# Optimization experiments

Measured on AMD Instinct MI355X. Metric: run time of the kernel, lower is better.

Reference implementation:

```python
import jax, jax.numpy as jnp
import numpy as np
from jax import lax


def conv(x, w, b, stride, pad):
    # x: [B,C,H,W], w: [O,I,kh,kw] (torch layout)
    y = lax.conv_general_dilated(x, w, (stride, stride), ((pad, pad), (pad, pad)),
                                 dimension_numbers=('NCHW', 'OIHW', 'NCHW'))
    return y + b[None, :, None, None]


def convT(x, w, b, stride, pad):
    # torch ConvTranspose2d weight layout [in, out, kh, kw]
    k = w.shape[2]
    wf = jnp.flip(w, (2, 3)).transpose(1, 0, 2, 3)  # -> [out, in, kh, kw]
    p = k - 1 - pad
    y = lax.conv_general_dilated(x, wf, (1, 1), ((p, p), (p, p)),
                                 lhs_dilation=(stride, stride),
                                 dimension_numbers=('NCHW', 'OIHW', 'NCHW'))
    return y + b[None, :, None, None]


def resblock(x, wa, ba, wb, bb):
    h = conv(jax.nn.relu(x), wa, ba, 1, 1)   # 3x3
    h2 = conv(jax.nn.relu(h), wb, bb, 1, 0)  # 1x1
    return x + h2


def vqvae_forward(x, e1_w, e1_b, e2_w, e2_b, e3_w, e3_b,
                  er1a_w, er1a_b, er1b_w, er1b_b, er2a_w, er2a_b, er2b_w, er2b_b,
                  codebook,
                  d1_w, d1_b, dr1a_w, dr1a_b, dr1b_w, dr1b_b,
                  dr2a_w, dr2a_b, dr2b_w, dr2b_b,
                  dt1_w, dt1_b, dt2_w, dt2_b):
    # encoder
    h = jax.nn.relu(conv(x, e1_w, e1_b, 2, 1))
    h = jax.nn.relu(conv(h, e2_w, e2_b, 2, 1))
    h = conv(h, e3_w, e3_b, 1, 1)
    h = resblock(h, er1a_w, er1a_b, er1b_w, er1b_b)
    ze = resblock(h, er2a_w, er2a_b, er2b_w, er2b_b)  # [B,C,H,W]
    # VQ: nearest codebook vector per spatial location (squared L2)
    zef = ze.transpose(0, 2, 3, 1)  # [B,H,W,C]
    # ||z - e||^2 = ||z||^2 - 2 z.e + ||e||^2 (same argmin as explicit broadcast)
    d = (jnp.sum(zef * zef, -1, keepdims=True)
         - 2.0 * jnp.einsum('bhwc,kc->bhwk', zef, codebook)
         + jnp.sum(codebook * codebook, -1))  # [B,H,W,K]
    idx = jnp.argmin(d, -1)                    # [B,H,W]
    zq = codebook[idx].transpose(0, 3, 1, 2)   # [B,C,H,W]
    # straight-through estimator
    dec_in = ze + lax.stop_gradient(zq - ze)
    # decoder
    g = conv(dec_in, d1_w, d1_b, 1, 1)
    g = resblock(g, dr1a_w, dr1a_b, dr1b_w, dr1b_b)
    g = resblock(g, dr2a_w, dr2a_b, dr2b_w, dr2b_b)
    g = jax.nn.relu(convT(g, dt1_w, dt1_b, 2, 1))
    x_hat = convT(g, dt2_w, dt2_b, 2, 1)
    return x_hat, ze, zq


def setup_inputs() -> dict:
    key = jax.random.key(0)
    ks = iter(jax.random.split(key, 64))
    C, K = 128, 512

    def w(shape, scale=0.02):
        return jax.random.normal(next(ks), shape, jnp.float32) * scale

    inp = {}
    inp['x'] = jax.random.normal(next(ks), (16, 3, 256, 256), jnp.float32)
    inp['e1_w'] = w((C, 3, 4, 4)); inp['e1_b'] = w((C,))
    inp['e2_w'] = w((C, C, 4, 4)); inp['e2_b'] = w((C,))
    inp['e3_w'] = w((C, C, 3, 3)); inp['e3_b'] = w((C,))
    inp['er1a_w'] = w((C, C, 3, 3)); inp['er1a_b'] = w((C,))
    inp['er1b_w'] = w((C, C, 1, 1)); inp['er1b_b'] = w((C,))
    inp['er2a_w'] = w((C, C, 3, 3)); inp['er2a_b'] = w((C,))
    inp['er2b_w'] = w((C, C, 1, 1)); inp['er2b_b'] = w((C,))
    inp['codebook'] = jax.random.uniform(next(ks), (K, C), jnp.float32, -1.0 / K, 1.0 / K)
    inp['d1_w'] = w((C, C, 3, 3)); inp['d1_b'] = w((C,))
    inp['dr1a_w'] = w((C, C, 3, 3)); inp['dr1a_b'] = w((C,))
    inp['dr1b_w'] = w((C, C, 1, 1)); inp['dr1b_b'] = w((C,))
    inp['dr2a_w'] = w((C, C, 3, 3)); inp['dr2a_b'] = w((C,))
    inp['dr2b_w'] = w((C, C, 1, 1)); inp['dr2b_b'] = w((C,))
    inp['dt1_w'] = w((C, C, 4, 4)); inp['dt1_b'] = w((C,))   # ConvTranspose [in,out,kh,kw]
    inp['dt2_w'] = w((C, 3, 4, 4)); inp['dt2_b'] = w((3,))
    return inp


def reference(x, e1_w, e1_b, e2_w, e2_b, e3_w, e3_b,
              er1a_w, er1a_b, er1b_w, er1b_b, er2a_w, er2a_b, er2b_w, er2b_b,
              codebook,
              d1_w, d1_b, dr1a_w, dr1a_b, dr1b_w, dr1b_b,
              dr2a_w, dr2a_b, dr2b_w, dr2b_b,
              dt1_w, dt1_b, dt2_w, dt2_b):
    return vqvae_forward(x, e1_w, e1_b, e2_w, e2_b, e3_w, e3_b,
                         er1a_w, er1a_b, er1b_w, er1b_b, er2a_w, er2a_b, er2b_w, er2b_b,
                         codebook,
                         d1_w, d1_b, dr1a_w, dr1a_b, dr1b_w, dr1b_b,
                         dr2a_w, dr2a_b, dr2b_w, dr2b_b,
                         dt1_w, dt1_b, dt2_w, dt2_b)
```

## Files before the change

### kernel.cpp

```cpp
#include <hip/hip_runtime.h>
#include <stdint.h>

typedef unsigned short u16;
typedef __attribute__((ext_vector_type(8))) short short8;
typedef __attribute__((ext_vector_type(4))) float floatx4;

#define RS66  (66*128)
#define IS66  (66*66*128)
#define RS130 (130*128)
#define IS130 (130*130*128)

__device__ __forceinline__ float bf2f(u16 h) {
  union { unsigned u; float f; } v; v.u = ((unsigned)h) << 16; return v.f;
}
__device__ __forceinline__ u16 f2bf(float f) {
  union { float f; unsigned u; } v; v.f = f;
  unsigned r = v.u + 0x7FFFu + ((v.u >> 16) & 1u);
  return (u16)(r >> 16);
}
__device__ __forceinline__ void gl_lds16(const void* g, void* l) {
  __builtin_amdgcn_global_load_lds(
      (const __attribute__((address_space(1))) void*)(uintptr_t)g,
      (__attribute__((address_space(3))) void*)(uintptr_t)l, 16, 0, 0);
}
__device__ __forceinline__ unsigned fkey(float f) {
  unsigned u = __float_as_uint(f);
  return (u & 0x80000000u) ? ~u : (u | 0x80000000u);
}

struct Taps { int n; unsigned dh2; unsigned dw2; };

__global__ __launch_bounds__(256) void conv_mfma(
    const u16* __restrict__ in, int inRS, int inIS, int si,
    const u16* __restrict__ wt, const float* __restrict__ bias, Taps tp,
    u16* __restrict__ out, int outRS, int outIS, int so, int oh0, int ow0,
    const u16* __restrict__ res, u16* __restrict__ out2, int reluMain,
    float* __restrict__ zeFc, u16* __restrict__ zeBFc, int multi)
{
  __shared__ u16 lA[4096];
  __shared__ u16 lB[4096];
  const int tid = threadIdx.x;
  const int w = tid >> 6, lane = tid & 63, quad = lane >> 4, l16 = lane & 15;
  const int wm = w >> 1, wn = w & 1;
  const int q = tid & 3, p0 = tid >> 2;
  const int blockM = blockIdx.x << 7;

  unsigned dh2 = tp.dh2, dw2 = tp.dw2;
  if (multi) {
    const int cls = blockIdx.y;
    dh2 = (tp.dh2 >> (8*cls)) & 0xffu;
    dw2 = (tp.dw2 >> (8*cls)) & 0xffu;
    wt += cls << 16;
    oh0 = cls >> 1; ow0 = cls & 1;
  }

  const int pg0 = blockM + p0, pg1 = pg0 + 64;
  const int b0 = pg0 >> 12, mo0 = (pg0 >> 6) & 63, no0 = pg0 & 63;
  const int b1 = pg1 >> 12, mo1 = (pg1 >> 6) & 63, no1 = pg1 & 63;
  const u16* gA0 = in + b0*inIS + si*mo0*inRS + si*no0*128 + q*8;
  const u16* gA1 = in + b1*inIS + si*mo1*inRS + si*no1*128 + q*8;
  const u16* gB0 = wt + p0*128 + q*8;
  const u16* gB1 = gB0 + 64*128;
  u16* lsA0 = lA + w*512; u16* lsA1 = lsA0 + 2048;
  u16* lsB0 = lB + w*512; u16* lsB1 = lsB0 + 2048;

  floatx4 zz = {0.f,0.f,0.f,0.f};
  floatx4 acc[4][4];
#pragma unroll
  for (int i=0;i<4;i++)
#pragma unroll
    for (int j=0;j<4;j++) acc[i][j] = zz;

  for (int t = 0; t < tp.n; ++t) {
    const int dh = (int)((dh2 >> (2*t)) & 3u) - 1;
    const int dw = (int)((dw2 >> (2*t)) & 3u) - 1;
    const int aoff = dh*inRS + dw*128;
    const int boff = t << 14;
#pragma unroll
    for (int kc = 0; kc < 4; ++kc) {
      __syncthreads();
      gl_lds16(gA0 + aoff + kc*32, lsA0);
      gl_lds16(gA1 + aoff + kc*32, lsA1);
      gl_lds16(gB0 + boff + kc*32, lsB0);
      gl_lds16(gB1 + boff + kc*32, lsB1);
      __syncthreads();
      short8 af[4], bfr[4];
#pragma unroll
      for (int s=0;s<4;s++) af[s]  = *(const short8*)&lA[(wm*64 + s*16 + l16)*32 + quad*8];
#pragma unroll
      for (int s=0;s<4;s++) bfr[s] = *(const short8*)&lB[(wn*64 + s*16 + l16)*32 + quad*8];
#pragma unroll
      for (int i=0;i<4;i++)
#pragma unroll
        for (int j=0;j<4;j++)
          acc[i][j] = __builtin_amdgcn_mfma_f32_16x16x32_bf16(af[i], bfr[j], acc[i][j], 0, 0, 0);
    }
  }

  float bv[4];
#pragma unroll
  for (int j=0;j<4;j++) bv[j] = bias[wn*64 + j*16 + l16];

#pragma unroll
  for (int i=0;i<4;i++) {
#pragma unroll
    for (int r=0;r<4;r++) {
      const int p = blockM + wm*64 + i*16 + quad*4 + r;
      const int bb = p >> 12, mo = (p >> 6) & 63, no = p & 63;
      const int ob = bb*outIS + (so*mo + oh0)*outRS + (so*no + ow0)*128;
#pragma unroll
      for (int j=0;j<4;j++) {
        const int n = wn*64 + j*16 + l16;
        float v = acc[i][j][r] + bv[j];
        if (res)  v += bf2f(res[ob + n]);
        if (out)  out[ob + n]  = f2bf(reluMain ? fmaxf(v, 0.f) : v);
        if (out2) out2[ob + n] = f2bf(fmaxf(v, 0.f));
        if (zeFc) {
          zeFc[((size_t)p << 7) + n] = v;
          zeBFc[((size_t)p << 7) + n] = f2bf(v);
        }
      }
    }
  }
}

__global__ __launch_bounds__(256) void vq_score(
    const u16* __restrict__ zeBF, const u16* __restrict__ cbBF,
    const float* __restrict__ cbn, unsigned long long* __restrict__ minbuf)
{
  __shared__ u16 lA[4096];
  __shared__ u16 lB[4096];
  const int tid = threadIdx.x;
  const int w = tid >> 6, lane = tid & 63, quad = lane >> 4, l16 = lane & 15;
  const int wm = w >> 1, wn = w & 1;
  const int q = tid & 3, p0 = tid >> 2;
  const int blockM = blockIdx.x << 7;
  const int nb = blockIdx.y;
  const u16* gA0 = zeBF + ((blockM + p0) << 7) + q*8;
  const u16* gA1 = gA0 + (64 << 7);
  const u16* gB0 = cbBF + ((nb*128 + p0) << 7) + q*8;
  const u16* gB1 = gB0 + (64 << 7);
  u16* lsA0 = lA + w*512; u16* lsA1 = lsA0 + 2048;
  u16* lsB0 = lB + w*512; u16* lsB1 = lsB0 + 2048;

  floatx4 zz = {0.f,0.f,0.f,0.f};
  floatx4 acc[4][4];
#pragma unroll
  for (int i=0;i<4;i++)
#pragma unroll
    for (int j=0;j<4;j++) acc[i][j] = zz;

#pragma unroll
  for (int kc = 0; kc < 4; ++kc) {
    __syncthreads();
    gl_lds16(gA0 + kc*32, lsA0);
    gl_lds16(gA1 + kc*32, lsA1);
    gl_lds16(gB0 + kc*32, lsB0);
    gl_lds16(gB1 + kc*32, lsB1);
    __syncthreads();
    short8 af[4], bfr[4];
#pragma unroll
    for (int s=0;s<4;s++) af[s]  = *(const short8*)&lA[(wm*64 + s*16 + l16)*32 + quad*8];
#pragma unroll
    for (int s=0;s<4;s++) bfr[s] = *(const short8*)&lB[(wn*64 + s*16 + l16)*32 + quad*8];
#pragma unroll
    for (int i=0;i<4;i++)
#pragma unroll
      for (int j=0;j<4;j++)
        acc[i][j] = __builtin_amdgcn_mfma_f32_16x16x32_bf16(af[i], bfr[j], acc[i][j], 0, 0, 0);
  }

  float cn[4];
#pragma unroll
  for (int j=0;j<4;j++) cn[j] = cbn[nb*128 + wn*64 + j*16 + l16];

#pragma unroll
  for (int i=0;i<4;i++) {
#pragma unroll
    for (int r=0;r<4;r++) {
      const int p = blockM + wm*64 + i*16 + quad*4 + r;
      unsigned long long best = 0xFFFFFFFFFFFFFFFFull;
#pragma unroll
      for (int j=0;j<4;j++) {
        const int n = nb*128 + wn*64 + j*16 + l16;
        float v = cn[j] - acc[i][j][r];
        unsigned long long pk = ((unsigned long long)fkey(v) << 32) | (unsigned)n;
        if (pk < best) best = pk;
      }
#pragma unroll
      for (int d=1; d<16; d<<=1) {
        unsigned long long o = __shfl_xor(best, d, 64);
        if (o < best) best = o;
      }
      if (l16 == 0) atomicMin(minbuf + p, best);
    }
  }
}

__global__ __launch_bounds__(256) void finalize(
    const float* __restrict__ zeFc, const unsigned long long* __restrict__ minb,
    const float* __restrict__ cb, float* __restrict__ outZe, float* __restrict__ outZq,
    u16* __restrict__ zqI)
{
  __shared__ float T[64*129];
  __shared__ int ns[64];
  const int tid = threadIdx.x;
  const int P0 = blockIdx.x << 6;
  const int b = P0 >> 12, hw0 = P0 & 4095;

#pragma unroll
  for (int it=0; it<32; ++it) {
    int e = it*256 + tid;
    int px = e >> 7, c = e & 127;
    T[px*129 + c] = zeFc[((size_t)P0 << 7) + e];
  }
  if (tid < 64) ns[tid] = (int)(unsigned)(minb[P0 + tid] & 0xFFFFFFFFull);
  __syncthreads();

  float* zeB = outZe + (((size_t)b) << 19) + hw0;
  float* zqB = outZq + (((size_t)b) << 19) + hw0;
  const int h = hw0 >> 6;
  u16* zqIB = zqI + b*IS66 + h*RS66;
#pragma unroll
  for (int it=0; it<32; ++it) {
    const int c = it*4 + (tid >> 6);
    const int px = tid & 63;
    zeB[(c << 12) + px] = T[px*129 + c];
    float v = cb[(ns[px] << 7) + c];
    zqB[(c << 12) + px] = v;
    zqIB[px*128 + c] = f2bf(v);
  }
}

__global__ __launch_bounds__(256) void zero_halos(
    u16* big, u16* s0, u16* s1, u16* s2, u16* s3, unsigned long long* minb)
{
  int id = blockIdx.x*256 + threadIdx.x;
  if (id >= 463872) return;
  if (id >= 398336) { minb[id - 398336] = 0xFFFFFFFFFFFFFFFFull; return; }
  u16* base; int H, W;
  if (id < 132096) { base = big; H = 128; W = 128; }
  else {
    id -= 132096;
    int bi = id / 66560;
    id -= bi*66560;
    base = (bi == 0) ? s0 : (bi == 1) ? s1 : (bi == 2) ? s2 : s3;
    H = 64; W = 64;
  }
  int Wp = W+2, Hp = H+2;
  int cv = id & 15; int rest = id >> 4;
  int npx = 2*Wp + 2*H;
  int img = rest / npx; int pix = rest - img*npx;
  int hh, wwp;
  if (pix < Wp) { hh = 0; wwp = pix; }
  else if (pix < 2*Wp) { hh = Hp-1; wwp = pix - Wp; }
  else { int r2 = pix - 2*Wp; hh = 1 + (r2 >> 1); wwp = (r2 & 1) ? (Wp-1) : 0; }
  uint4 zv = {0u,0u,0u,0u};
  *(uint4*)(base + (((size_t)img*Hp + hh)*Wp + wwp)*128 + cv*8) = zv;
}

struct WEnt { const float* src; u16* dst; int O, I, T, mode; };
struct WTab { int n; WEnt e[16]; int cum[17]; };
__global__ __launch_bounds__(256) void prep_w(WTab wt) {
  int id = blockIdx.x*256 + threadIdx.x;
  if (id >= wt.cum[wt.n]) return;
  int k = 0;
  while (id >= wt.cum[k+1]) k++;
  int l = id - wt.cum[k];
  WEnt E = wt.e[k];
  if (E.mode == 0) {
    int i = l % E.I; int rest = l / E.I; int o = rest % E.O; int t = rest / E.O;
    E.dst[l] = f2bf(E.src[(o*E.I + i)*E.T + t]);
  } else if (E.mode == 1) {
    int i = l & 127, o = (l >> 7) & 127, tt = (l >> 14) & 3, cls = l >> 16;
    int th = tt >> 1, tw = tt & 1, po = cls >> 1, pw = cls & 1;
    int kh = po ? (th ? 2 : 0) : (th ? 3 : 1);
    int kw = pw ? (tw ? 2 : 0) : (tw ? 3 : 1);
    E.dst[l] = f2bf(E.src[((i*128 + o)*4 + kh)*4 + kw]);
  } else if (E.mode == 2) {
    E.dst[l] = f2bf(E.src[l]);
  } else if (E.mode == 3) {
    float s = 0.f; const float* r = E.src + l*128;
    for (int c=0;c<128;c++) s += r[c]*r[c];
    ((float*)E.dst)[l] = 0.5f*s;
  } else if (E.mode == 4) {
    int o = l & 127, tap = l >> 7;
    ((float*)E.dst)[l] = E.src[o*48 + tap];
  } else {
    int c = l & 127, n = l >> 7;
    int o = n >> 4, kk = n & 15;
    E.dst[l] = f2bf(E.src[c*48 + o*16 + kk]);
  }
}

__global__ __launch_bounds__(256) void conv_e1(
    const float* __restrict__ x, const float* __restrict__ wT,
    const float* __restrict__ bias, u16* __restrict__ outI)
{
  __shared__ float inS[12*260];
  __shared__ float wS[48*128];
  __shared__ float bS[128];
  const int tid = threadIdx.x;
  const int b = blockIdx.x >> 7, ho = blockIdx.x & 127;

  for (int l = tid; l < 1536; l += 256)
    ((float4*)wS)[l] = ((const float4*)wT)[l];
  if (tid < 128) bS[tid] = bias[tid];
  for (int l = tid; l < 3120; l += 256) {
    int col = l % 260; int rest = l / 260;
    int kh = rest & 3, c = rest >> 2;
    int hi = 2*ho + kh - 1, wi = col - 1;
    float v = 0.f;
    if ((unsigned)hi < 256u && (unsigned)wi < 256u)
      v = x[((b*3 + c) << 16) + (hi << 8) + wi];
    inS[rest*260 + col] = v;
  }
  __syncthreads();

  const int g = tid & 7;
  const int pxg = tid >> 3;
  floatx4 acc[4][4];
  {
    const floatx4* bp = (const floatx4*)&bS[g*16];
    floatx4 b0 = bp[0], b1 = bp[1], b2 = bp[2], b3 = bp[3];
#pragma unroll
    for (int px=0;px<4;px++) { acc[px][0]=b0; acc[px][1]=b1; acc[px][2]=b2; acc[px][3]=b3; }
  }
#pragma unroll
  for (int c=0;c<3;c++)
#pragma unroll
    for (int kh=0;kh<4;kh++) {
      const float* row = &inS[(c*4+kh)*260];
#pragma unroll
      for (int kw=0;kw<4;kw++) {
        const int tap = c*16 + kh*4 + kw;
        const floatx4* wp = (const floatx4*)&wS[tap*128 + g*16];
        floatx4 w0 = wp[0], w1 = wp[1], w2 = wp[2], w3 = wp[3];
#pragma unroll
        for (int px=0;px<4;px++) {
          float xv = row[((pxg*4 + px) << 1) + kw];
          acc[px][0] += xv*w0; acc[px][1] += xv*w1;
          acc[px][2] += xv*w2; acc[px][3] += xv*w3;
        }
      }
    }

  u16* ob = outI + b*IS130 + ho*RS130;
#pragma unroll
  for (int px=0;px<4;px++) {
    const int wo = pxg*4 + px;
    u16* p = ob + wo*128 + g*16;
#pragma unroll
    for (int k=0;k<4;k++) {
      union { u16 u[4]; uint2 v2; } pk;
#pragma unroll
      for (int j=0;j<4;j++) pk.u[j] = f2bf(fmaxf(acc[px][k][j], 0.f));
      *(uint2*)(p + k*4) = pk.v2;
    }
  }
}

__global__ __launch_bounds__(256) void dt2_gemm(
    const u16* __restrict__ inI, const u16* __restrict__ Wb,
    float* __restrict__ cols)
{
  const int tid = threadIdx.x;
  const int w = tid >> 6, lane = tid & 63, quad = lane >> 4, l16 = lane & 15;
  const int pixBase = blockIdx.x*256 + w*64;

  short8 Bf[3][4];
#pragma unroll
  for (int nt=0; nt<3; nt++)
#pragma unroll
    for (int kc=0; kc<4; kc++)
      Bf[nt][kc] = *(const short8*)(Wb + (nt*16 + l16)*128 + kc*32 + quad*8);

  const u16* ap[4];
#pragma unroll
  for (int ms=0; ms<4; ms++) {
    int p = pixBase + ms*16 + l16;
    int b = p >> 14, rem = p & 16383;
    ap[ms] = inI + b*IS130 + (rem >> 7)*RS130 + (rem & 127)*128;
  }

  floatx4 zz = {0.f,0.f,0.f,0.f};
  floatx4 acc[4][3];
#pragma unroll
  for (int ms=0; ms<4; ms++)
#pragma unroll
    for (int nt=0; nt<3; nt++) acc[ms][nt] = zz;

#pragma unroll
  for (int kc=0; kc<4; kc++) {
#pragma unroll
    for (int ms=0; ms<4; ms++) {
      short8 a = *(const short8*)(ap[ms] + kc*32 + quad*8);
#pragma unroll
      for (int nt=0; nt<3; nt++)
        acc[ms][nt] = __builtin_amdgcn_mfma_f32_16x16x32_bf16(a, Bf[nt][kc], acc[ms][nt], 0, 0, 0);
    }
  }

#pragma unroll
  for (int ms=0; ms<4; ms++)
#pragma unroll
    for (int nt=0; nt<3; nt++)
#pragma unroll
      for (int r=0; r<4; r++) {
        int p = pixBase + ms*16 + quad*4 + r;
        cols[(size_t)p*48 + nt*16 + l16] = acc[ms][nt][r];
      }
}

__global__ __launch_bounds__(256) void dt2_gather(
    const float* __restrict__ cols, const float* __restrict__ bias,
    float* __restrict__ xhat)
{
  int id = blockIdx.x*256 + threadIdx.x;
  int b = id >> 16, rem = id & 65535;
  int ho = rem >> 8, wo = rem & 255;
  const int ph = ho & 1, pw = wo & 1;
  const int hi0 = ph ? ((ho+1)>>1) : (ho>>1);
  const int kh0 = ph ? 0 : 1;
  const int wi0 = pw ? ((wo+1)>>1) : (wo>>1);
  const int kw0 = pw ? 0 : 1;
  float a0 = bias[0], a1 = bias[1], a2 = bias[2];
#pragma unroll
  for (int th=0; th<2; th++) {
    const int hi = hi0 - th;
    if ((unsigned)hi >= 128u) continue;
    const int kh = kh0 + 2*th;
#pragma unroll
    for (int tw=0; tw<2; tw++) {
      const int wi = wi0 - tw;
      if ((unsigned)wi >= 128u) continue;
      const int kw = kw0 + 2*tw;
      const float* r = cols + (size_t)((b << 14) + (hi << 7) + wi)*48 + (kh*4 + kw);
      a0 += r[0]; a1 += r[16]; a2 += r[32];
    }
  }
  const int ob = ((b*3) << 16) + (ho << 8) + wo;
  xhat[ob]          = a0;
  xhat[ob + 65536]  = a1;
  xhat[ob + 131072] = a2;
}

extern "C" void kernel_launch(void* const* d_in, const int* in_sizes, int n_in,
                              void* d_out, int out_size, void* d_ws, size_t ws_size,
                              hipStream_t stream)
{
  const float* x     = (const float*)d_in[0];
  const float* e1w   = (const float*)d_in[1];
  const float* e1b   = (const float*)d_in[2];
  const float* e2w   = (const float*)d_in[3];
  const float* e2b   = (const float*)d_in[4];
  const float* e3w   = (const float*)d_in[5];
  const float* e3b   = (const float*)d_in[6];
  const float* er1aw = (const float*)d_in[7];
  const float* er1ab = (const float*)d_in[8];
  const float* er1bw = (const float*)d_in[9];
  const float* er1bb = (const float*)d_in[10];
  const float* er2aw = (const float*)d_in[11];
  const float* er2ab = (const float*)d_in[12];
  const float* er2bw = (const float*)d_in[13];
  const float* er2bb = (const float*)d_in[14];
  const float* cb    = (const float*)d_in[15];
  const float* d1w   = (const float*)d_in[16];
  const float* d1b   = (const float*)d_in[17];
  const float* dr1aw = (const float*)d_in[18];
  const float* dr1ab = (const float*)d_in[19];
  const float* dr1bw = (const float*)d_in[20];
  const float* dr1bb = (const float*)d_in[21];
  const float* dr2aw = (const float*)d_in[22];
  const float* dr2ab = (const float*)d_in[23];
  const float* dr2bw = (const float*)d_in[24];
  const float* dr2bb = (const float*)d_in[25];
  const float* dt1w  = (const float*)d_in[26];
  const float* dt1b  = (const float*)d_in[27];
  const float* dt2w  = (const float*)d_in[28];
  const float* dt2b  = (const float*)d_in[29];
  float* out = (float*)d_out;

  char* ws = (char*)d_ws;
  size_t off = 0;
  auto alloc = [&](size_t bytes) -> void* {
    void* r = ws + off; off += (bytes + 255) & ~(size_t)255; return r;
  };

  u16* BIG = (u16*)alloc((size_t)IS130*16*2);
  u16* S[4];
  for (int i=0;i<4;i++) S[i] = (u16*)alloc((size_t)IS66*16*2);
  unsigned long long* minb = (unsigned long long*)alloc((size_t)65536*8);
  u16* W_e2 = (u16*)alloc(262144*2);
  u16* W9[6]; for (int i=0;i<6;i++) W9[i] = (u16*)alloc(147456*2);
  u16* W1[4]; for (int i=0;i<4;i++) W1[i] = (u16*)alloc(16384*2);
  u16* Wdt1 = (u16*)alloc(262144*2);
  u16* cbBF = (u16*)alloc(65536*2);
  float* cbn = (float*)alloc(512*4);
  float* wsE1 = (float*)alloc(6144*4);
  u16* Wb48 = (u16*)alloc(6144*2);

  u16* BIGi = BIG + RS130 + 128;
  u16* Si[4];
  for (int i=0;i<4;i++) Si[i] = S[i] + RS66 + 128;
  u16* zeBFc = S[1];
  float* zeFc = (float*)BIG;
  float* cols = (float*)S[1];

  zero_halos<<<1812, 256, 0, stream>>>(BIG, S[0], S[1], S[2], S[3], minb);

  WTab wtab; int ne = 0; wtab.cum[0] = 0;
  auto addw = [&](const float* s, u16* d, int O, int I, int T, int m, int items) {
    wtab.e[ne] = {s, d, O, I, T, m};
    wtab.cum[ne+1] = wtab.cum[ne] + items; ne++;
  };
  addw(e2w,   W_e2, 128,128,16,0, 262144);
  addw(e3w,   W9[0],128,128, 9,0, 147456);
  addw(er1aw, W9[1],128,128, 9,0, 147456);
  addw(er2aw, W9[2],128,128, 9,0, 147456);
  addw(d1w,   W9[3],128,128, 9,0, 147456);
  addw(dr1aw, W9[4],128,128, 9,0, 147456);
  addw(dr2aw, W9[5],128,128, 9,0, 147456);
  addw(er1bw, W1[0],128,128, 1,0, 16384);
  addw(er2bw, W1[1],128,128, 1,0, 16384);
  addw(dr1bw, W1[2],128,128, 1,0, 16384);
  addw(dr2bw, W1[3],128,128, 1,0, 16384);
  addw(dt1w,  Wdt1, 0,0,0,1, 262144);
  addw(cb,    cbBF, 0,0,0,2, 65536);
  addw(cb,    (u16*)cbn, 0,0,0,3, 512);
  addw(e1w,   (u16*)wsE1, 0,0,0,4, 6144);
  addw(dt2w,  Wb48, 0,0,0,5, 6144);
  wtab.n = ne;
  prep_w<<<(wtab.cum[ne] + 255)/256, 256, 0, stream>>>(wtab);

  conv_e1<<<2048, 256, 0, stream>>>(x, wsE1, e1b, BIGi);

  Taps t16; t16.n = 16; t16.dh2 = 0; t16.dw2 = 0;
  for (int t=0;t<16;t++) { t16.dh2 |= (unsigned)(t>>2) << (2*t); t16.dw2 |= (unsigned)(t&3) << (2*t); }
  Taps t9; t9.n = 9; t9.dh2 = 0; t9.dw2 = 0;
  for (int t=0;t<9;t++) { t9.dh2 |= (unsigned)(t/3) << (2*t); t9.dw2 |= (unsigned)(t%3) << (2*t); }
  Taps t1x; t1x.n = 1; t1x.dh2 = 1; t1x.dw2 = 1;
  Taps tcm; tcm.n = 4; tcm.dh2 = 0; tcm.dw2 = 0;
  for (int cls=0; cls<4; ++cls) {
    int po = cls >> 1, pw = cls & 1;
    for (int tt=0; tt<4; ++tt) {
      int th = tt >> 1, tw = tt & 1;
      int dh = po ? (th ? 0 : 1) : (th ? -1 : 0);
      int dw = pw ? (tw ? 0 : 1) : (tw ? -1 : 0);
      tcm.dh2 |= (unsigned)(dh+1) << (8*cls + 2*tt);
      tcm.dw2 |= (unsigned)(dw+1) << (8*cls + 2*tt);
    }
  }

  auto conv = [&](const u16* in_, int iRS, int iIS, int si,
                  const u16* w_, const float* b_, Taps tp,
                  u16* o_, int oRS, int oIS, int so, int oh, int ow,
                  const u16* r_, u16* o2, int rl, float* zf, u16* zb) {
    conv_mfma<<<512, 256, 0, stream>>>(in_, iRS, iIS, si, w_, b_, tp,
                                       o_, oRS, oIS, so, oh, ow, r_, o2, rl, zf, zb, 0);
  };

  conv(BIGi, RS130, IS130, 2, W_e2, e2b, t16, Si[0], RS66, IS66, 1,0,0, nullptr, nullptr, 1, nullptr, nullptr);
  conv(Si[0], RS66, IS66, 1, W9[0], e3b, t9, Si[1], RS66, IS66, 1,0,0, nullptr, Si[2], 0, nullptr, nullptr);
  conv(Si[2], RS66, IS66, 1, W9[1], er1ab, t9, Si[0], RS66, IS66, 1,0,0, nullptr, nullptr, 1, nullptr, nullptr);
  conv(Si[0], RS66, IS66, 1, W1[0], er1bb, t1x, Si[3], RS66, IS66, 1,0,0, Si[1], Si[2], 0, nullptr, nullptr);
  conv(Si[2], RS66, IS66, 1, W9[2], er2ab, t9, Si[0], RS66, IS66, 1,0,0, nullptr, nullptr, 1, nullptr, nullptr);
  conv(Si[0], RS66, IS66, 1, W1[1], er2bb, t1x, nullptr, RS66, IS66, 1,0,0, Si[3], nullptr, 0, zeFc, zeBFc);

  vq_score<<<dim3(512,4), 256, 0, stream>>>(zeBFc, cbBF, cbn, minb);
  finalize<<<1024, 256, 0, stream>>>(zeFc, minb, cb, out + 3145728, out + 11534336, Si[2]);

  conv(Si[2], RS66, IS66, 1, W9[3], d1b, t9, Si[0], RS66, IS66, 1,0,0, nullptr, Si[1], 0, nullptr, nullptr);
  conv(Si[1], RS66, IS66, 1, W9[4], dr1ab, t9, Si[2], RS66, IS66, 1,0,0, nullptr, nullptr, 1, nullptr, nullptr);
  conv(Si[2], RS66, IS66, 1, W1[2], dr1bb, t1x, Si[3], RS66, IS66, 1,0,0, Si[0], Si[1], 0, nullptr, nullptr);
  conv(Si[1], RS66, IS66, 1, W9[5], dr2ab, t9, Si[2], RS66, IS66, 1,0,0, nullptr, nullptr, 1, nullptr, nullptr);
  conv(Si[2], RS66, IS66, 1, W1[3], dr2bb, t1x, Si[0], RS66, IS66, 1,0,0, Si[3], nullptr, 0, nullptr, nullptr);

  conv_mfma<<<dim3(512,4), 256, 0, stream>>>(Si[0], RS66, IS66, 1, Wdt1, dt1b, tcm,
                                             BIGi, RS130, IS130, 2, 0, 0,
                                             nullptr, nullptr, 1, nullptr, nullptr, 1);

  dt2_gemm<<<1024, 256, 0, stream>>>(BIGi, Wb48, cols);
  dt2_gather<<<4096, 256, 0, stream>>>(cols, dt2b, out);
}
```

Before: 747.2 us.

## Double-buffer conv MFMA LDS tiles with larger K chunks and XOR swizzle

The conv GEMM main loop now keeps two LDS buffers and prefetches the next K chunk with global_load_lds while MFMAs run on the current one, with one barrier per chunk instead of two. The K chunk grows from 32 to 64 channels. Rows are XOR-swizzled to avoid LDS bank conflicts on fragment reads. The trade-off is that LDS use per block rises from 16 KB to 64 KB, which may limit how many blocks fit on each CU.

After: 710.3 us. -4.9%, faster.

```diff
diff --git a/kernel.cpp b/kernel.cpp
--- a/kernel.cpp
+++ b/kernel.cpp
@@ -37,12 +37,11 @@
     const u16* __restrict__ res, u16* __restrict__ out2, int reluMain,
     float* __restrict__ zeFc, u16* __restrict__ zeBFc, int multi)
 {
-  __shared__ u16 lA[4096];
-  __shared__ u16 lB[4096];
+  __shared__ u16 lA[2][8192];
+  __shared__ u16 lB[2][8192];
   const int tid = threadIdx.x;
   const int w = tid >> 6, lane = tid & 63, quad = lane >> 4, l16 = lane & 15;
   const int wm = w >> 1, wn = w & 1;
-  const int q = tid & 3, p0 = tid >> 2;
   const int blockM = blockIdx.x << 7;
 
   unsigned dh2 = tp.dh2, dw2 = tp.dw2;
@@ -54,15 +53,16 @@
     oh0 = cls >> 1; ow0 = cls & 1;
   }
 
-  const int pg0 = blockM + p0, pg1 = pg0 + 64;
-  const int b0 = pg0 >> 12, mo0 = (pg0 >> 6) & 63, no0 = pg0 & 63;
-  const int b1 = pg1 >> 12, mo1 = (pg1 >> 6) & 63, no1 = pg1 & 63;
-  const u16* gA0 = in + b0*inIS + si*mo0*inRS + si*no0*128 + q*8;
-  const u16* gA1 = in + b1*inIS + si*mo1*inRS + si*no1*128 + q*8;
-  const u16* gB0 = wt + p0*128 + q*8;
-  const u16* gB1 = gB0 + 64*128;
-  u16* lsA0 = lA + w*512; u16* lsA1 = lsA0 + 2048;
-  u16* lsB0 = lB + w*512; u16* lsB1 = lsB0 + 2048;
+  const int swz = (tid & 7) ^ ((tid >> 3) & 7);
+  const u16* gA[4]; const u16* gB[4];
+#pragma unroll
+  for (int i=0;i<4;i++) {
+    const int pg = blockM + i*32 + (tid >> 3);
+    const int b = pg >> 12, mo = (pg >> 6) & 63, no = pg & 63;
+    gA[i] = in + b*inIS + si*mo*inRS + si*no*128 + swz*8;
+    gB[i] = wt + (i*32 + (tid >> 3))*128 + swz*8;
+  }
+  const int ldsOff = w*512;
 
   floatx4 zz = {0.f,0.f,0.f,0.f};
   floatx4 acc[4][4];
@@ -71,24 +71,39 @@
 #pragma unroll
     for (int j=0;j<4;j++) acc[i][j] = zz;
 
-  for (int t = 0; t < tp.n; ++t) {
+  const int NCH = tp.n << 1;
+  auto issue = [&](int ci, int buf) {
+    const int t = ci >> 1, kc = ci & 1;
     const int dh = (int)((dh2 >> (2*t)) & 3u) - 1;
     const int dw = (int)((dw2 >> (2*t)) & 3u) - 1;
-    const int aoff = dh*inRS + dw*128;
-    const int boff = t << 14;
-#pragma unroll
-    for (int kc = 0; kc < 4; ++kc) {
-      __syncthreads();
-      gl_lds16(gA0 + aoff + kc*32, lsA0);
-      gl_lds16(gA1 + aoff + kc*32, lsA1);
-      gl_lds16(gB0 + boff + kc*32, lsB0);
-      gl_lds16(gB1 + boff + kc*32, lsB1);
-      __syncthreads();
+    const int aoff = dh*inRS + dw*128 + kc*64;
+    const int boff = (t << 14) + kc*64;
+#pragma unroll
+    for (int i=0;i<4;i++) {
+      gl_lds16(gA[i] + aoff, &lA[buf][i*2048 + ldsOff]);
+      gl_lds16(gB[i] + boff, &lB[buf][i*2048 + ldsOff]);
+    }
+  };
+
+  issue(0, 0);
+  for (int ci = 0; ci < NCH; ++ci) {
+    __syncthreads();
+    if (ci + 1 < NCH) issue(ci + 1, (ci + 1) & 1);
+    const u16* bufA = lA[ci & 1];
+    const u16* bufB = lB[ci & 1];
+#pragma unroll
+    for (int kk=0; kk<2; ++kk) {
       short8 af[4], bfr[4];
 #pragma unroll
-      for (int s=0;s<4;s++) af[s]  = *(const short8*)&lA[(wm*64 + s*16 + l16)*32 + quad*8];
-#pragma unroll
-      for (int s=0;s<4;s++) bfr[s] = *(const short8*)&lB[(wn*64 + s*16 + l16)*32 + quad*8];
+      for (int s=0;s<4;s++) {
+        const int row = wm*64 + s*16 + l16;
+        af[s]  = *(const short8*)&bufA[row*64 + (((kk*4 + quad) ^ (l16 & 7)) << 3)];
+      }
+#pragma unroll
+      for (int s=0;s<4;s++) {
+        const int row = wn*64 + s*16 + l16;
+        bfr[s] = *(const short8*)&bufB[row*64 + (((kk*4 + quad) ^ (l16 & 7)) << 3)];
+      }
 #pragma unroll
       for (int i=0;i<4;i++)
 #pragma unroll
```
